# Kernel tuning notes

Hardware: AMD Instinct MI355X
Metric: run time of the kernel (lower is better)

The kernel has to match this reference:

```python
import jax, jax.numpy as jnp
import numpy as np

B, T, IN, H, NCLS = 128, 512, 4, 256, 3


def _lstm_dir(x_tbi, w_ih, w_hh, b, reverse):
    """One direction of one LSTM layer. x_tbi: [T,B,in] -> ys [T,B,H].
    Gate order matches torch: i, f, g, o."""
    # Precompute input projections for all timesteps (one big GEMM).
    xp = jnp.einsum('tbi,gi->tbg', x_tbi, w_ih) + b  # [T,B,4H]
    nB = x_tbi.shape[1]
    nH = w_hh.shape[1]
    h0 = jnp.zeros((nB, nH), x_tbi.dtype)
    c0 = jnp.zeros((nB, nH), x_tbi.dtype)

    def step(carry, gx):
        h, c = carry
        g = gx + h @ w_hh.T  # [B,4H]
        i, f, gg, o = jnp.split(g, 4, axis=-1)
        c = jax.nn.sigmoid(f) * c + jax.nn.sigmoid(i) * jnp.tanh(gg)
        h = jax.nn.sigmoid(o) * jnp.tanh(c)
        return (h, c), h

    _, ys = jax.lax.scan(step, (h0, c0), xp, reverse=reverse)
    return ys  # [T,B,H], time-aligned with input for both directions


def _bilstm_layer(x_tbi, w_ih, w_hh, b):
    yf = _lstm_dir(x_tbi, w_ih[0], w_hh[0], b[0], reverse=False)
    yb = _lstm_dir(x_tbi, w_ih[1], w_hh[1], b[1], reverse=True)
    return jnp.concatenate([yf, yb], axis=-1)  # [T,B,2H]


def setup_inputs() -> dict:
    key = jax.random.key(0)
    ks = jax.random.split(key, 9)
    s = 0.05
    return {
        'x': jax.random.normal(ks[0], (B, T, IN), jnp.float32),
        'w_ih_l0': jax.random.normal(ks[1], (2, 4 * H, IN), jnp.float32) * s,
        'w_hh_l0': jax.random.normal(ks[2], (2, 4 * H, H), jnp.float32) * s,
        'b_l0': jax.random.normal(ks[3], (2, 4 * H), jnp.float32) * s,
        'w_ih_l1': jax.random.normal(ks[4], (2, 4 * H, 2 * H), jnp.float32) * s,
        'w_hh_l1': jax.random.normal(ks[5], (2, 4 * H, H), jnp.float32) * s,
        'b_l1': jax.random.normal(ks[6], (2, 4 * H), jnp.float32) * s,
        'w_out': jax.random.normal(ks[7], (NCLS, H), jnp.float32) * s,
        'b_out': jax.random.normal(ks[8], (NCLS,), jnp.float32) * s,
    }


def reference(x, w_ih_l0, w_hh_l0, b_l0, w_ih_l1, w_hh_l1, b_l1, w_out, b_out):
    xt = jnp.transpose(x, (1, 0, 2))  # [T,B,4] (time-major for scan)
    b0 = b_l0[:, None, :]  # broadcast over [T,B]
    b1 = b_l1[:, None, :]
    y0 = _bilstm_layer(xt, w_ih_l0, w_hh_l0, b0)   # [T,B,2H]
    y1 = _bilstm_layer(y0, w_ih_l1, w_hh_l1, b1)   # [T,B,2H]
    # sum directions, then take last timestep (torch: out[:,:,:H]+out[:,:,H:], out[:,-1,:])
    last = y1[-1, :, :H] + y1[-1, :, H:]           # [B,H]
    logits = last @ w_out.T + b_out                # [B,3]
    return jax.nn.softmax(logits, axis=1)
```

## Files before the change

### kernel.cpp

```cpp
#include <hip/hip_runtime.h>

typedef __attribute__((ext_vector_type(8))) short bf16x8;
typedef __attribute__((ext_vector_type(4))) float f32x4;
typedef __attribute__((ext_vector_type(4))) int   i32x4;

#define T_LEN 512
#define BATCH 128
#define HID   256
#define G4    1024
#define WPI8_STRIDE 262144
#define L2E   1.4426950408889634f

__device__ __forceinline__ float sigmf(float x){
  return __builtin_amdgcn_rcpf(1.0f + __expf(-x));
}
__device__ __forceinline__ float tanhf_(float x){
  return 1.0f - 2.0f*__builtin_amdgcn_rcpf(1.0f + __expf(2.0f*x));
}
__device__ __forceinline__ float sig2(float y){
  return __builtin_amdgcn_rcpf(1.0f + __builtin_amdgcn_exp2f(-y));
}
__device__ __forceinline__ float tanh2(float y){
  return 1.0f - 2.0f*__builtin_amdgcn_rcpf(1.0f + __builtin_amdgcn_exp2f(y));
}
__device__ __forceinline__ unsigned short f2bf(float f){
  union{float f;unsigned u;} v; v.f=f;
  unsigned r = v.u + 0x7FFF + ((v.u>>16)&1);
  return (unsigned short)(r>>16);
}
__device__ __forceinline__ float bf2f(unsigned short b){
  union{unsigned u;float f;} v; v.u = ((unsigned)b)<<16; return v.f;
}

__global__ void k_scales(const float* __restrict__ w_hh0, const float* __restrict__ w_hh1,
                         float* __restrict__ comb, float* __restrict__ s_inv){
  int idx = blockIdx.x*256 + threadIdx.x;
  if (idx >= 3*1024) return;
  int dl = idx >> 10, n = idx & 1023;
  const float* src = (dl < 2) ? (w_hh0 + ((size_t)dl*1024 + n)*256)
                              : (w_hh1 + (size_t)n*256);
  float m = 1e-20f;
  for (int k = 0; k < 256; k += 4){
    float4 v = *(const float4*)&src[k];
    m = fmaxf(m, fmaxf(fmaxf(fabsf(v.x), fabsf(v.y)), fmaxf(fabsf(v.z), fabsf(v.w))));
  }
  s_inv[idx] = 127.f / m;
  comb[idx]  = m / 16129.f;
}

__global__ void k_pack_i8(const float* __restrict__ w_hh0, const float* __restrict__ w_hh1,
                          const float* __restrict__ s_inv, char* __restrict__ wp){
  int idx = blockIdx.x*256 + threadIdx.x;
  if (idx >= 3*WPI8_STRIDE) return;
  int j    = idx & 15;
  int lane = (idx >> 4) & 63;
  int kk   = (idx >> 10) & 3;
  int tile = (idx >> 12) & 63;
  int dl   = idx >> 18;
  int g = tile & 3, s = tile >> 2;
  int n = g*256 + s*16 + (lane & 15);
  int k = kk*64 + ((lane >> 4) << 4) + j;
  const float* src = (dl < 2) ? (w_hh0 + ((size_t)dl*1024 + n)*256)
                              : (w_hh1 + (size_t)n*256);
  float v = src[k] * s_inv[dl*1024 + n];
  int q = (int)rintf(fminf(127.f, fmaxf(-127.f, v)));
  wp[idx] = (char)q;
}

__global__ void k_pack_wih1(const float* __restrict__ w, const float* __restrict__ b1,
                            unsigned short* __restrict__ o, float* __restrict__ b1perm){
  int idx = blockIdx.x*256 + threadIdx.x;
  if (idx >= 2*1024*512) return;
  int d     = idx >> 19;
  int rem   = idx & ((1 << 19) - 1);
  int n_out = rem >> 9;
  int k     = rem & 511;
  int n_src = d ? n_out
                : ((n_out & 3)*256 + (n_out >> 6)*16 + ((n_out >> 2) & 15));
  o[idx] = f2bf(w[((size_t)(d*1024 + n_src))*512 + k]);
  if (idx < 1024){
    int ns = (idx & 3)*256 + (idx >> 6)*16 + ((idx >> 2) & 15);
    b1perm[idx] = b1[ns];
  }
}

template<int MODE>
__global__ __launch_bounds__(512, 2) void k_rec2(
    const float* __restrict__ x,
    const char* __restrict__ wpack,
    const float* __restrict__ comb,
    const float* __restrict__ w_ih0,
    const float* __restrict__ b0,
    const unsigned short* __restrict__ xp,
    unsigned short* __restrict__ y0,
    float* __restrict__ hS)
{
  const int tid  = threadIdx.x;
  const int lane = tid & 63;
  const int w    = tid >> 6;
  int dir, bgrp, dl;
  if (MODE == 0){ dir = blockIdx.x >> 6; bgrp = blockIdx.x & 63; dl = dir; }
  else          { dir = 0; bgrp = blockIdx.x; dl = 2; }
  const int b0r = bgrp * 2;

  __shared__ __align__(16) char   A_lds[2][2*288];
  __shared__ __align__(16) float  x_lds[2][2][4];

  const i32x4* wpb = (const i32x4*)(wpack + (size_t)dl*WPI8_STRIDE);
  i32x4 breg[2][4][4];
  #pragma unroll
  for (int p = 0; p < 2; ++p)
    #pragma unroll
    for (int g = 0; g < 4; ++g)
      #pragma unroll
      for (int kk = 0; kk < 4; ++kk)
        breg[p][g][kk] = wpb[(((((2*w+p)*4 + g)*4) + kk) << 6) + lane];

  const int c  = lane & 15;
  const int bl = (lane >> 4) & 1;
  const int pl = lane >> 5;
  const int jc = (2*w + pl)*16 + c;

  const float FOLD[4] = {L2E, L2E, 2.f*L2E, L2E};

  float cmb_l[4];
  #pragma unroll
  for (int g = 0; g < 4; ++g)
    cmb_l[g] = comb[dl*1024 + g*256 + jc] * FOLD[g];

  float4 wvr[4]; float biar[4];
  if (MODE == 0){
    #pragma unroll
    for (int g = 0; g < 4; ++g){
      float4 wv4 = *(const float4*)&w_ih0[(size_t)(dir*1024 + g*256 + jc)*4];
      wv4.x *= FOLD[g]; wv4.y *= FOLD[g]; wv4.z *= FOLD[g]; wv4.w *= FOLD[g];
      wvr[g]  = wv4;
      biar[g] = b0[dir*1024 + g*256 + jc] * FOLD[g];
    }
  }

  for (int i = tid; i < 2*2*288; i += 512) ((char*)A_lds)[i] = 0;
  if (MODE == 0 && tid < 8){
    int row = tid >> 2, i = tid & 3;
    int t0 = dir ? (T_LEN-1) : 0;
    x_lds[0][row][i] = x[((size_t)(b0r+row)*T_LEN + t0)*4 + i];
  }

  float c_reg = 0.f;

  uint2 cinC, cinN;
  if (MODE == 1)
    cinC = *(const uint2*)&xp[((((size_t)0*64 + bgrp)*8 + w)*64 + lane)*4];

  for (int tt = 0; tt < T_LEN; ++tt){
    const int t = (MODE == 0 && dir) ? (T_LEN-1-tt) : tt;
    const char* Ac = A_lds[tt & 1];
    char* An = (char*)A_lds[(tt + 1) & 1];

    __syncthreads();

    i32x4 a[4];
    #pragma unroll
    for (int kk = 0; kk < 4; ++kk)
      a[kk] = *(const i32x4*)&Ac[(c & 1)*288 + kk*64 + ((lane >> 4) << 4)];

    if (MODE == 1){
      int tn = (t + 1 < T_LEN) ? t + 1 : t;
      cinN = *(const uint2*)&xp[((((size_t)tn*64 + bgrp)*8 + w)*64 + lane)*4];
    }

    i32x4 acc[2][4];
    #pragma unroll
    for (int p = 0; p < 2; ++p)
      #pragma unroll
      for (int g = 0; g < 4; ++g){
        acc[p][g] = (i32x4){0,0,0,0};
        #pragma unroll
        for (int kk = 0; kk < 4; ++kk)
          acc[p][g] = __builtin_amdgcn_mfma_i32_16x16x64_i8(a[kk], breg[p][g][kk], acc[p][g], 0, 0, 0);
      }

    float4 xr;
    if (MODE == 0) xr = *(const float4*)&x_lds[tt & 1][bl][0];

    float gv[4];
    #pragma unroll
    for (int g = 0; g < 4; ++g){
      int a0 = bl ? acc[0][g][1] : acc[0][g][0];
      int a1 = bl ? acc[1][g][1] : acc[1][g][0];
      int ia = pl ? a1 : a0;
      if (MODE == 0){
        float t0 = fmaf(xr.x, wvr[g].x, biar[g]);
        t0 = fmaf(xr.y, wvr[g].y, t0);
        t0 = fmaf(xr.z, wvr[g].z, t0);
        t0 = fmaf(xr.w, wvr[g].w, t0);
        gv[g] = fmaf((float)ia, cmb_l[g], t0);
      } else {
        unsigned uu = (g < 2) ? cinC.x : cinC.y;
        float ci = bf2f((unsigned short)((g & 1) ? (uu >> 16) : (uu & 0xFFFF)));
        gv[g] = fmaf((float)ia, cmb_l[g], ci);
      }
    }
    float cc = sig2(gv[1])*c_reg + sig2(gv[0])*tanh2(gv[2]);
    c_reg = cc;
    float h = sig2(gv[3])*tanhf_(cc);
    float hcl = fminf(127.f, fmaxf(-127.f, h*127.f));
    An[bl*288 + jc] = (char)__float2int_rn(hcl);

    if (MODE == 0){
      unsigned pk;
      asm("v_cvt_pk_bf16_f32 %0, %1, %2" : "=v"(pk) : "v"(h), "v"(h));
      y0[((size_t)t*BATCH + (b0r + bl))*(2*HID) + dir*HID + jc] = (unsigned short)pk;
    } else if (tt == T_LEN-1){
      hS[(size_t)(b0r + bl)*HID + jc] = h;
    }

    if (MODE == 0 && tid < 8){
      int tn = dir ? (t > 0 ? t-1 : 0) : (t < T_LEN-1 ? t+1 : t);
      int row = tid >> 2, i = tid & 3;
      x_lds[(tt + 1) & 1][row][i] = x[((size_t)(b0r+row)*T_LEN + tn)*4 + i];
    }
    if (MODE == 1) cinC = cinN;
  }
}

template<int PLAIN>
__global__ __launch_bounds__(256) void k_gemm_bf(
    const unsigned short* __restrict__ A, const unsigned short* __restrict__ B,
    const float* __restrict__ bias, unsigned short* __restrict__ outF, float* __restrict__ outP)
{
  __shared__ __align__(16) unsigned short As[128*64];
  __shared__ __align__(16) unsigned short Bs[128*64];
  const int tid  = threadIdx.x;
  const int lane = tid & 63;
  const int w = tid >> 6, wm = w >> 1, wn = w & 1;
  const int t  = blockIdx.y;
  const int n0 = blockIdx.x * 128;

  f32x4 acc[4][4];
  #pragma unroll
  for (int i = 0; i < 4; ++i)
    #pragma unroll
    for (int jx = 0; jx < 4; ++jx) acc[i][jx] = (f32x4){0.f,0.f,0.f,0.f};

  const int sr = tid >> 3;
  const int sq = tid & 7;

  for (int k0 = 0; k0 < 512; k0 += 64){
    #pragma unroll
    for (int it = 0; it < 4; ++it){
      int r = sr + it*32;
      uint4 av = *(const uint4*)&A[((size_t)t*128 + r)*512 + k0 + sq*8];
      uint4 bv = *(const uint4*)&B[((size_t)(n0 + r))*512 + k0 + sq*8];
      *(uint4*)&As[r*64 + (sq ^ (r & 7))*8] = av;
      *(uint4*)&Bs[r*64 + (sq ^ (r & 7))*8] = bv;
    }
    __syncthreads();
    bf16x8 af[4][2], bfv[4][2];
    #pragma unroll
    for (int mt = 0; mt < 4; ++mt)
      #pragma unroll
      for (int kk = 0; kk < 2; ++kk){
        int row = wm*64 + mt*16 + (lane & 15);
        af[mt][kk] = *(const bf16x8*)&As[row*64 + ((kk*4 + (lane>>4)) ^ (row & 7))*8];
      }
    #pragma unroll
    for (int nl = 0; nl < 4; ++nl)
      #pragma unroll
      for (int kk = 0; kk < 2; ++kk){
        int row = wn*64 + nl*16 + (lane & 15);
        bfv[nl][kk] = *(const bf16x8*)&Bs[row*64 + ((kk*4 + (lane>>4)) ^ (row & 7))*8];
      }
    #pragma unroll
    for (int mt = 0; mt < 4; ++mt)
      #pragma unroll
      for (int nl = 0; nl < 4; ++nl){
        acc[mt][nl] = __builtin_amdgcn_mfma_f32_16x16x32_bf16(af[mt][0], bfv[nl][0], acc[mt][nl], 0,0,0);
        acc[mt][nl] = __builtin_amdgcn_mfma_f32_16x16x32_bf16(af[mt][1], bfv[nl][1], acc[mt][nl], 0,0,0);
      }
    __syncthreads();
  }

  #pragma unroll
  for (int mt = 0; mt < 4; ++mt){
    #pragma unroll
    for (int nl = 0; nl < 4; ++nl){
      int ng = n0 + wn*64 + nl*16 + (lane & 15);
      float bv = bias[ng];
      f32x4 v = acc[mt][nl];
      if (PLAIN){
        int mrow = wm*64 + mt*16 + (lane >> 4)*4;
        #pragma unroll
        for (int r = 0; r < 4; ++r)
          outP[((size_t)t*128 + mrow + r)*G4 + ng] = v[r] + bv;
      } else {
        int g  = ng & 3;
        int cc = (ng >> 2) & 15;
        int s  = ng >> 6;
        float fold = (g == 2) ? (2.f*L2E) : L2E;
        int mrow = wm*64 + mt*16 + ((lane >> 4) << 2);
        #pragma unroll
        for (int r = 0; r < 4; ++r){
          int m  = mrow + r;
          int bg = m >> 1, bb = m & 1;
          outF[((((size_t)t*64 + bg)*8 + (s >> 1))*64
                + (((s & 1) << 5) | (bb << 4) | cc))*4 + g] = f2bf((v[r] + bv)*fold);
        }
      }
    }
  }
}

__global__ __launch_bounds__(256) void k_final(const float* __restrict__ hS,
                                               const float* __restrict__ xp1b,
                                               const float* __restrict__ w_out,
                                               const float* __restrict__ b_out,
                                               float* __restrict__ out)
{
  const int b = blockIdx.x, j = threadIdx.x;
  float iv = xp1b[b*G4 + 0*HID + j];
  float gv = xp1b[b*G4 + 2*HID + j];
  float ov = xp1b[b*G4 + 3*HID + j];
  float c  = sigmf(iv)*tanhf_(gv);
  float hb = sigmf(ov)*tanhf_(c);
  float last = hS[b*HID + j] + hb;

  __shared__ float part[3][256];
  part[0][j] = last * w_out[0*HID + j];
  part[1][j] = last * w_out[1*HID + j];
  part[2][j] = last * w_out[2*HID + j];
  __syncthreads();
  for (int s = 128; s > 0; s >>= 1){
    if (j < s){
      part[0][j] += part[0][j+s];
      part[1][j] += part[1][j+s];
      part[2][j] += part[2][j+s];
    }
    __syncthreads();
  }
  if (j == 0){
    float l0 = part[0][0] + b_out[0];
    float l1 = part[1][0] + b_out[1];
    float l2 = part[2][0] + b_out[2];
    float m = fmaxf(l0, fmaxf(l1, l2));
    float e0 = __expf(l0-m), e1 = __expf(l1-m), e2 = __expf(l2-m);
    float s = e0 + e1 + e2;
    out[b*3+0] = e0/s; out[b*3+1] = e1/s; out[b*3+2] = e2/s;
  }
}

extern "C" void kernel_launch(void* const* d_in, const int* in_sizes, int n_in,
                              void* d_out, int out_size, void* d_ws, size_t ws_size,
                              hipStream_t stream) {
  const float* x     = (const float*)d_in[0];
  const float* w_ih0 = (const float*)d_in[1];
  const float* w_hh0 = (const float*)d_in[2];
  const float* b0p   = (const float*)d_in[3];
  const float* w_ih1 = (const float*)d_in[4];
  const float* w_hh1 = (const float*)d_in[5];
  const float* b1p   = (const float*)d_in[6];
  const float* w_out = (const float*)d_in[7];
  const float* b_out = (const float*)d_in[8];
  float* out = (float*)d_out;

  unsigned short* y0    = (unsigned short*)d_ws;
  unsigned short* xp1   = y0    + (size_t)T_LEN*BATCH*2*HID;
  unsigned short* wih1p = xp1   + (size_t)T_LEN*BATCH*G4;
  float*          comb  = (float*)(wih1p + 2*G4*2*HID);
  float*          s_inv = comb  + 3*1024;
  float*          b1pm  = s_inv + 3*1024;
  float*          xp1b  = b1pm  + 1024;
  float*          hS    = xp1b  + BATCH*G4;
  char*           wpi8  = (char*)(hS + BATCH*HID);

  k_scales<<<12, 256, 0, stream>>>(w_hh0, w_hh1, comb, s_inv);
  k_pack_i8<<<3072, 256, 0, stream>>>(w_hh0, w_hh1, s_inv, wpi8);
  k_pack_wih1<<<4096, 256, 0, stream>>>(w_ih1, b1p, wih1p, b1pm);

  k_rec2<0><<<128, 512, 0, stream>>>(x, wpi8, comb, w_ih0, b0p, nullptr, y0, nullptr);

  k_gemm_bf<0><<<dim3(8, 512), 256, 0, stream>>>(y0, wih1p, b1pm, xp1, nullptr);

  k_gemm_bf<1><<<dim3(8, 1), 256, 0, stream>>>(y0 + (size_t)(T_LEN-1)*BATCH*2*HID,
                                               wih1p + (size_t)G4*2*HID, b1p + G4,
                                               nullptr, xp1b);

  k_rec2<1><<<64, 512, 0, stream>>>(nullptr, wpi8, comb, nullptr, nullptr, xp1, nullptr, hS);

  k_final<<<BATCH, 256, 0, stream>>>(hS, xp1b, w_out, b_out, out);
}
```

Measured before the change: 994.3 us.

## Overlap layer-1 input-projection GEMM with layer-1 recurrence via chunked atomic counters

Fuses the layer-1 input GEMM and the layer-1 forward recurrence into one launch. 128 blocks compute the GEMM in 64-timestep chunks and signal completion through agent-scope atomic counters. 64 other blocks run the recurrence and spin-wait on each chunk's counter before consuming it. The goal is to hide the big GEMM behind the latency-bound sequential scan. The costs are a memset, spin-waiting, and a dependence on all 192 blocks being co-resident to avoid deadlock.

```diff
diff --git a/kernel.cpp b/kernel.cpp
--- a/kernel.cpp
+++ b/kernel.cpp
@@ -84,27 +84,24 @@
   }
 }
 
-template<int MODE>
-__global__ __launch_bounds__(512, 2) void k_rec2(
+__global__ __launch_bounds__(512, 2) void k_rec0(
     const float* __restrict__ x,
     const char* __restrict__ wpack,
     const float* __restrict__ comb,
     const float* __restrict__ w_ih0,
     const float* __restrict__ b0,
-    const unsigned short* __restrict__ xp,
-    unsigned short* __restrict__ y0,
-    float* __restrict__ hS)
+    unsigned short* __restrict__ y0)
 {
   const int tid  = threadIdx.x;
   const int lane = tid & 63;
   const int w    = tid >> 6;
-  int dir, bgrp, dl;
-  if (MODE == 0){ dir = blockIdx.x >> 6; bgrp = blockIdx.x & 63; dl = dir; }
-  else          { dir = 0; bgrp = blockIdx.x; dl = 2; }
-  const int b0r = bgrp * 2;
-
-  __shared__ __align__(16) char   A_lds[2][2*288];
-  __shared__ __align__(16) float  x_lds[2][2][4];
+  const int dir  = blockIdx.x >> 6;
+  const int bgrp = blockIdx.x & 63;
+  const int dl   = dir;
+  const int b0r  = bgrp * 2;
+
+  __shared__ __align__(16) char  A_lds[2][2*288];
+  __shared__ __align__(16) float x_lds[2][2][4];
 
   const i32x4* wpb = (const i32x4*)(wpack + (size_t)dl*WPI8_STRIDE);
   i32x4 breg[2][4][4];
@@ -122,25 +119,22 @@
   const int jc = (2*w + pl)*16 + c;
 
   const float FOLD[4] = {L2E, L2E, 2.f*L2E, L2E};
-
   float cmb_l[4];
   #pragma unroll
   for (int g = 0; g < 4; ++g)
     cmb_l[g] = comb[dl*1024 + g*256 + jc] * FOLD[g];
 
   float4 wvr[4]; float biar[4];
-  if (MODE == 0){
-    #pragma unroll
-    for (int g = 0; g < 4; ++g){
-      float4 wv4 = *(const float4*)&w_ih0[(size_t)(dir*1024 + g*256 + jc)*4];
-      wv4.x *= FOLD[g]; wv4.y *= FOLD[g]; wv4.z *= FOLD[g]; wv4.w *= FOLD[g];
-      wvr[g]  = wv4;
-      biar[g] = b0[dir*1024 + g*256 + jc] * FOLD[g];
-    }
+  #pragma unroll
+  for (int g = 0; g < 4; ++g){
+    float4 wv4 = *(const float4*)&w_ih0[(size_t)(dir*1024 + g*256 + jc)*4];
+    wv4.x *= FOLD[g]; wv4.y *= FOLD[g]; wv4.z *= FOLD[g]; wv4.w *= FOLD[g];
+    wvr[g]  = wv4;
+    biar[g] = b0[dir*1024 + g*256 + jc] * FOLD[g];
   }
 
   for (int i = tid; i < 2*2*288; i += 512) ((char*)A_lds)[i] = 0;
-  if (MODE == 0 && tid < 8){
+  if (tid < 8){
     int row = tid >> 2, i = tid & 3;
     int t0 = dir ? (T_LEN-1) : 0;
     x_lds[0][row][i] = x[((size_t)(b0r+row)*T_LEN + t0)*4 + i];
@@ -148,12 +142,8 @@
 
   float c_reg = 0.f;
 
-  uint2 cinC, cinN;
-  if (MODE == 1)
-    cinC = *(const uint2*)&xp[((((size_t)0*64 + bgrp)*8 + w)*64 + lane)*4];
-
   for (int tt = 0; tt < T_LEN; ++tt){
-    const int t = (MODE == 0 && dir) ? (T_LEN-1-tt) : tt;
+    const int t = dir ? (T_LEN-1-tt) : tt;
     const char* Ac = A_lds[tt & 1];
     char* An = (char*)A_lds[(tt + 1) & 1];
 
@@ -163,11 +153,6 @@
     #pragma unroll
     for (int kk = 0; kk < 4; ++kk)
       a[kk] = *(const i32x4*)&Ac[(c & 1)*288 + kk*64 + ((lane >> 4) << 4)];
-
-    if (MODE == 1){
-      int tn = (t + 1 < T_LEN) ? t + 1 : t;
-      cinN = *(const uint2*)&xp[((((size_t)tn*64 + bgrp)*8 + w)*64 + lane)*4];
-    }
 
     i32x4 acc[2][4];
     #pragma unroll
@@ -180,8 +165,7 @@
           acc[p][g] = __builtin_amdgcn_mfma_i32_16x16x64_i8(a[kk], breg[p][g][kk], acc[p][g], 0, 0, 0);
       }
 
-    float4 xr;
-    if (MODE == 0) xr = *(const float4*)&x_lds[tt & 1][bl][0];
+    float4 xr = *(const float4*)&x_lds[tt & 1][bl][0];
 
     float gv[4];
     #pragma unroll
@@ -189,17 +173,11 @@
       int a0 = bl ? acc[0][g][1] : acc[0][g][0];
       int a1 = bl ? acc[1][g][1] : acc[1][g][0];
       int ia = pl ? a1 : a0;
-      if (MODE == 0){
-        float t0 = fmaf(xr.x, wvr[g].x, biar[g]);
-        t0 = fmaf(xr.y, wvr[g].y, t0);
-        t0 = fmaf(xr.z, wvr[g].z, t0);
-        t0 = fmaf(xr.w, wvr[g].w, t0);
-        gv[g] = fmaf((float)ia, cmb_l[g], t0);
-      } else {
-        unsigned uu = (g < 2) ? cinC.x : cinC.y;
-        float ci = bf2f((unsigned short)((g & 1) ? (uu >> 16) : (uu & 0xFFFF)));
-        gv[g] = fmaf((float)ia, cmb_l[g], ci);
-      }
+      float t0 = fmaf(xr.x, wvr[g].x, biar[g]);
+      t0 = fmaf(xr.y, wvr[g].y, t0);
+      t0 = fmaf(xr.z, wvr[g].z, t0);
+      t0 = fmaf(xr.w, wvr[g].w, t0);
+      gv[g] = fmaf((float)ia, cmb_l[g], t0);
     }
     float cc = sig2(gv[1])*c_reg + sig2(gv[0])*tanh2(gv[2]);
     c_reg = cc;
@@ -207,27 +185,215 @@
     float hcl = fminf(127.f, fmaxf(-127.f, h*127.f));
     An[bl*288 + jc] = (char)__float2int_rn(hcl);
 
-    if (MODE == 0){
-      unsigned pk;
-      asm("v_cvt_pk_bf16_f32 %0, %1, %2" : "=v"(pk) : "v"(h), "v"(h));
-      y0[((size_t)t*BATCH + (b0r + bl))*(2*HID) + dir*HID + jc] = (unsigned short)pk;
-    } else if (tt == T_LEN-1){
-      hS[(size_t)(b0r + bl)*HID + jc] = h;
-    }
-
-    if (MODE == 0 && tid < 8){
+    unsigned pk;
+    asm("v_cvt_pk_bf16_f32 %0, %1, %2" : "=v"(pk) : "v"(h), "v"(h));
+    y0[((size_t)t*BATCH + (b0r + bl))*(2*HID) + dir*HID + jc] = (unsigned short)pk;
+
+    if (tid < 8){
       int tn = dir ? (t > 0 ? t-1 : 0) : (t < T_LEN-1 ? t+1 : t);
       int row = tid >> 2, i = tid & 3;
       x_lds[(tt + 1) & 1][row][i] = x[((size_t)(b0r+row)*T_LEN + tn)*4 + i];
     }
-    if (MODE == 1) cinC = cinN;
-  }
-}
-
-template<int PLAIN>
-__global__ __launch_bounds__(256) void k_gemm_bf(
+  }
+}
+
+__global__ __launch_bounds__(512, 2) void k_l1_fused(
+    const unsigned short* __restrict__ y0,
+    const unsigned short* __restrict__ B,
+    const float* __restrict__ bias,
+    unsigned short* __restrict__ xp,
+    const char* __restrict__ wpack,
+    const float* __restrict__ comb,
+    float* __restrict__ hS,
+    unsigned* __restrict__ cnt)
+{
+  __shared__ __align__(16) unsigned short As[2][128*64];
+  __shared__ __align__(16) unsigned short Bs[2][128*64];
+  __shared__ __align__(16) char A_lds[2][2*288];
+
+  const int bx = blockIdx.x;
+
+  if (bx < 128){
+    const int tid5 = threadIdx.x;
+    const int sub  = tid5 >> 8;
+    const int tid  = tid5 & 255;
+    const int lane = tid & 63;
+    const int w = tid >> 6, wm = w >> 1, wn = w & 1;
+    const int sr = tid >> 3, sq = tid & 7;
+    const int worker = bx*2 + sub;
+
+    for (int cch = 0; cch < 8; ++cch){
+      for (int j = worker; j < 512; j += 256){
+        const int t  = cch*64 + (j >> 3);
+        const int n0 = (j & 7) * 128;
+
+        f32x4 acc[4][4];
+        #pragma unroll
+        for (int i = 0; i < 4; ++i)
+          #pragma unroll
+          for (int jx = 0; jx < 4; ++jx) acc[i][jx] = (f32x4){0.f,0.f,0.f,0.f};
+
+        for (int k0 = 0; k0 < 512; k0 += 64){
+          #pragma unroll
+          for (int it = 0; it < 4; ++it){
+            int r = sr + it*32;
+            uint4 av = *(const uint4*)&y0[((size_t)t*128 + r)*512 + k0 + sq*8];
+            uint4 bv = *(const uint4*)&B[((size_t)(n0 + r))*512 + k0 + sq*8];
+            *(uint4*)&As[sub][r*64 + (sq ^ (r & 7))*8] = av;
+            *(uint4*)&Bs[sub][r*64 + (sq ^ (r & 7))*8] = bv;
+          }
+          __syncthreads();
+          bf16x8 af[4][2], bfv[4][2];
+          #pragma unroll
+          for (int mt = 0; mt < 4; ++mt)
+            #pragma unroll
+            for (int kk = 0; kk < 2; ++kk){
+              int row = wm*64 + mt*16 + (lane & 15);
+              af[mt][kk] = *(const bf16x8*)&As[sub][row*64 + ((kk*4 + (lane>>4)) ^ (row & 7))*8];
+            }
+          #pragma unroll
+          for (int nl = 0; nl < 4; ++nl)
+            #pragma unroll
+            for (int kk = 0; kk < 2; ++kk){
+              int row = wn*64 + nl*16 + (lane & 15);
+              bfv[nl][kk] = *(const bf16x8*)&Bs[sub][row*64 + ((kk*4 + (lane>>4)) ^ (row & 7))*8];
+            }
+          #pragma unroll
+          for (int mt = 0; mt < 4; ++mt)
+            #pragma unroll
+            for (int nl = 0; nl < 4; ++nl){
+              acc[mt][nl] = __builtin_amdgcn_mfma_f32_16x16x32_bf16(af[mt][0], bfv[nl][0], acc[mt][nl], 0,0,0);
+              acc[mt][nl] = __builtin_amdgcn_mfma_f32_16x16x32_bf16(af[mt][1], bfv[nl][1], acc[mt][nl], 0,0,0);
+            }
+          __syncthreads();
+        }
+
+        #pragma unroll
+        for (int mt = 0; mt < 4; ++mt){
+          #pragma unroll
+          for (int nl = 0; nl < 4; ++nl){
+            int ng = n0 + wn*64 + nl*16 + (lane & 15);
+            float bv = bias[ng];
+            f32x4 v = acc[mt][nl];
+            int g   = ng & 3;
+            int ccx = (ng >> 2) & 15;
+            int s   = ng >> 6;
+            float fold = (g == 2) ? (2.f*L2E) : L2E;
+            int mrow = wm*64 + mt*16 + ((lane >> 4) << 2);
+            #pragma unroll
+            for (int r = 0; r < 4; ++r){
+              int m  = mrow + r;
+              int bg = m >> 1, bb = m & 1;
+              xp[((((size_t)t*64 + bg)*8 + (s >> 1))*64
+                  + (((s & 1) << 5) | (bb << 4) | ccx))*4 + g] = f2bf((v[r] + bv)*fold);
+            }
+          }
+        }
+      }
+      asm volatile("s_waitcnt vmcnt(0)" ::: "memory");
+      __syncthreads();
+      if (tid == 0)
+        __hip_atomic_fetch_add(&cnt[cch], 2u, __ATOMIC_RELEASE, __HIP_MEMORY_SCOPE_AGENT);
+    }
+    return;
+  }
+
+  const int tid  = threadIdx.x;
+  const int lane = tid & 63;
+  const int w    = tid >> 6;
+  const int bgrp = bx - 128;
+  const int b0r  = bgrp * 2;
+
+  const i32x4* wpb = (const i32x4*)(wpack + (size_t)2*WPI8_STRIDE);
+  i32x4 breg[2][4][4];
+  #pragma unroll
+  for (int p = 0; p < 2; ++p)
+    #pragma unroll
+    for (int g = 0; g < 4; ++g)
+      #pragma unroll
+      for (int kk = 0; kk < 4; ++kk)
+        breg[p][g][kk] = wpb[(((((2*w+p)*4 + g)*4) + kk) << 6) + lane];
+
+  const int c  = lane & 15;
+  const int bl = (lane >> 4) & 1;
+  const int pl = lane >> 5;
+  const int jc = (2*w + pl)*16 + c;
+
+  const float FOLD[4] = {L2E, L2E, 2.f*L2E, L2E};
+  float cmb_l[4];
+  #pragma unroll
+  for (int g = 0; g < 4; ++g)
+    cmb_l[g] = comb[2*1024 + g*256 + jc] * FOLD[g];
+
+  for (int i = tid; i < 2*2*288; i += 512) ((char*)A_lds)[i] = 0;
+
+  float c_reg = 0.f;
+
+  if (tid == 0)
+    while (__hip_atomic_load(&cnt[0], __ATOMIC_ACQUIRE, __HIP_MEMORY_SCOPE_AGENT) < 512u) {}
+  __syncthreads();
+
+  uint2 cinC, cinN;
+  cinC = *(const uint2*)&xp[((((size_t)0*64 + bgrp)*8 + w)*64 + lane)*4];
+
+  for (int tt = 0; tt < T_LEN; ++tt){
+    const int t = tt;
+    const char* Ac = A_lds[tt & 1];
+    char* An = (char*)A_lds[(tt + 1) & 1];
+
+    if (tid == 0 && tt < T_LEN-1 && (tt & 63) == 63){
+      int cn = (tt + 1) >> 6;
+      while (__hip_atomic_load(&cnt[cn], __ATOMIC_ACQUIRE, __HIP_MEMORY_SCOPE_AGENT) < 512u) {}
+    }
+    __syncthreads();
+
+    i32x4 a[4];
+    #pragma unroll
+    for (int kk = 0; kk < 4; ++kk)
+      a[kk] = *(const i32x4*)&Ac[(c & 1)*288 + kk*64 + ((lane >> 4) << 4)];
+
+    {
+      int tn = (t + 1 < T_LEN) ? t + 1 : t;
+      cinN = *(const uint2*)&xp[((((size_t)tn*64 + bgrp)*8 + w)*64 + lane)*4];
+    }
+
+    i32x4 acc[2][4];
+    #pragma unroll
+    for (int p = 0; p < 2; ++p)
+      #pragma unroll
+      for (int g = 0; g < 4; ++g){
+        acc[p][g] = (i32x4){0,0,0,0};
+        #pragma unroll
+        for (int kk = 0; kk < 4; ++kk)
+          acc[p][g] = __builtin_amdgcn_mfma_i32_16x16x64_i8(a[kk], breg[p][g][kk], acc[p][g], 0, 0, 0);
+      }
+
+    float gv[4];
+    #pragma unroll
+    for (int g = 0; g < 4; ++g){
+      int a0 = bl ? acc[0][g][1] : acc[0][g][0];
+      int a1 = bl ? acc[1][g][1] : acc[1][g][0];
+      int ia = pl ? a1 : a0;
+      unsigned uu = (g < 2) ? cinC.x : cinC.y;
+      float ci = bf2f((unsigned short)((g & 1) ? (uu >> 16) : (uu & 0xFFFF)));
+      gv[g] = fmaf((float)ia, cmb_l[g], ci);
+    }
+    float cc = sig2(gv[1])*c_reg + sig2(gv[0])*tanh2(gv[2]);
+    c_reg = cc;
+    float h = sig2(gv[3])*tanhf_(cc);
+    float hcl = fminf(127.f, fmaxf(-127.f, h*127.f));
+    An[bl*288 + jc] = (char)__float2int_rn(hcl);
+
+    if (tt == T_LEN-1)
+      hS[(size_t)(b0r + bl)*HID + jc] = h;
+
+    cinC = cinN;
+  }
+}
+
+__global__ __launch_bounds__(256) void k_gemm_plain(
     const unsigned short* __restrict__ A, const unsigned short* __restrict__ B,
-    const float* __restrict__ bias, unsigned short* __restrict__ outF, float* __restrict__ outP)
+    const float* __restrict__ bias, float* __restrict__ outP)
 {
   __shared__ __align__(16) unsigned short As[128*64];
   __shared__ __align__(16) unsigned short Bs[128*64];
@@ -288,25 +454,10 @@
       int ng = n0 + wn*64 + nl*16 + (lane & 15);
       float bv = bias[ng];
       f32x4 v = acc[mt][nl];
-      if (PLAIN){
-        int mrow = wm*64 + mt*16 + (lane >> 4)*4;
-        #pragma unroll
-        for (int r = 0; r < 4; ++r)
-          outP[((size_t)t*128 + mrow + r)*G4 + ng] = v[r] + bv;
-      } else {
-        int g  = ng & 3;
-        int cc = (ng >> 2) & 15;
-        int s  = ng >> 6;
-        float fold = (g == 2) ? (2.f*L2E) : L2E;
-        int mrow = wm*64 + mt*16 + ((lane >> 4) << 2);
-        #pragma unroll
-        for (int r = 0; r < 4; ++r){
-          int m  = mrow + r;
-          int bg = m >> 1, bb = m & 1;
-          outF[((((size_t)t*64 + bg)*8 + (s >> 1))*64
-                + (((s & 1) << 5) | (bb << 4) | cc))*4 + g] = f2bf((v[r] + bv)*fold);
-        }
-      }
+      int mrow = wm*64 + mt*16 + (lane >> 4)*4;
+      #pragma unroll
+      for (int r = 0; r < 4; ++r)
+        outP[((size_t)t*128 + mrow + r)*G4 + ng] = v[r] + bv;
     }
   }
 }
@@ -372,20 +523,19 @@
   float*          xp1b  = b1pm  + 1024;
   float*          hS    = xp1b  + BATCH*G4;
   char*           wpi8  = (char*)(hS + BATCH*HID);
+  unsigned*       cnt   = (unsigned*)(wpi8 + 3*WPI8_STRIDE);
 
   k_scales<<<12, 256, 0, stream>>>(w_hh0, w_hh1, comb, s_inv);
   k_pack_i8<<<3072, 256, 0, stream>>>(w_hh0, w_hh1, s_inv, wpi8);
   k_pack_wih1<<<4096, 256, 0, stream>>>(w_ih1, b1p, wih1p, b1pm);
 
-  k_rec2<0><<<128, 512, 0, stream>>>(x, wpi8, comb, w_ih0, b0p, nullptr, y0, nullptr);
-
-  k_gemm_bf<0><<<dim3(8, 512), 256, 0, stream>>>(y0, wih1p, b1pm, xp1, nullptr);
-
-  k_gemm_bf<1><<<dim3(8, 1), 256, 0, stream>>>(y0 + (size_t)(T_LEN-1)*BATCH*2*HID,
-                                               wih1p + (size_t)G4*2*HID, b1p + G4,
-                                               nullptr, xp1b);
-
-  k_rec2<1><<<64, 512, 0, stream>>>(nullptr, wpi8, comb, nullptr, nullptr, xp1, nullptr, hS);
+  k_rec0<<<128, 512, 0, stream>>>(x, wpi8, comb, w_ih0, b0p, y0);
+
+  k_gemm_plain<<<dim3(8, 1), 256, 0, stream>>>(y0 + (size_t)(T_LEN-1)*BATCH*2*HID,
+                                               wih1p + (size_t)G4*2*HID, b1p + G4, xp1b);
+
+  hipMemsetAsync(cnt, 0, 8*sizeof(unsigned), stream);
+  k_l1_fused<<<192, 512, 0, stream>>>(y0, wih1p, b1pm, xp1, wpi8, comb, hS, cnt);
 
   k_final<<<BATCH, 256, 0, stream>>>(hS, xp1b, w_out, b_out, out);
 }
```

Result: no change. 984.2 us (-1.0%).
